# Kernel tuning notes

Measured on AMD Instinct MI355X. Metric: run time of the kernel, lower is better.

## Reference

```python
import jax, jax.numpy as jnp
import numpy as np

EPS = 1e-8  # matches torch cosine_similarity eps


def setup_inputs() -> dict:
    key = jax.random.key(0)
    ks = jax.random.split(key, 8)
    B, D_IN, H, L = 256, 256, 256, 100000
    G = 5 * H  # (N_GATES + 1) * hidden_dim
    s_in = 1.0 / np.sqrt(D_IN)
    s_h = 1.0 / np.sqrt(H)
    return {
        "x_t": jax.random.normal(ks[0], (B, D_IN), jnp.float32),
        "h": jax.random.normal(ks[1], (B, H), jnp.float32),
        "c": jax.random.normal(ks[2], (B, H), jnp.float32),
        "W_i2h": jax.random.normal(ks[3], (G, D_IN), jnp.float32) * s_in,
        "b_i2h": jnp.zeros((G,), jnp.float32),
        "W_h2h": jax.random.normal(ks[4], (G, H), jnp.float32) * s_h,
        "b_h2h": jnp.zeros((G,), jnp.float32),
        "keys": jax.random.normal(ks[5], (L, D_IN), jnp.float32),
        "vals": jax.random.normal(ks[6], (L, H), jnp.float32),
    }


def _dnd_get_memory(q, keys, vals):
    # cosine similarity of each query against every stored key -> [B, L]
    qn = q / jnp.maximum(jnp.linalg.norm(q, axis=-1, keepdims=True), EPS)
    kn = keys / jnp.maximum(jnp.linalg.norm(keys, axis=-1, keepdims=True), EPS)
    sims = jnp.einsum("bd,ld->bl", qn, kn)
    w = jax.nn.softmax(sims, axis=-1)          # softmax-weighted aggregation
    return jnp.einsum("bl,lh->bh", w, vals)    # [B, H]


def reference(x_t, h, c, W_i2h, b_i2h, W_h2h, b_h2h, keys, vals):
    H = h.shape[1]
    preact = (x_t @ W_i2h.T + b_i2h) + (h @ W_h2h.T + b_h2h)   # [B, 5H]
    gates = jax.nn.sigmoid(preact[:, : 4 * H])
    f_t = gates[:, :H]
    i_t = gates[:, H:2 * H]
    o_t = gates[:, 2 * H:3 * H]
    r_t = gates[:, 3 * H:4 * H]
    c_t_new = jnp.tanh(preact[:, 4 * H:])
    c_t = f_t * c + i_t * c_t_new
    m_t = jnp.tanh(_dnd_get_memory(x_t, keys, vals))
    c_t = c_t + r_t * m_t
    h_t = o_t * jnp.tanh(c_t)
    return (h_t, c_t)
```

## Files before the change

### kernel.cpp

```cpp
#include <hip/hip_runtime.h>
#include <stdint.h>

typedef float f4_t __attribute__((ext_vector_type(4)));
typedef float f16_t __attribute__((ext_vector_type(16)));
typedef __bf16 bf8_t __attribute__((ext_vector_type(8)));
typedef unsigned short us4_t __attribute__((ext_vector_type(4)));
typedef unsigned short us8_t __attribute__((ext_vector_type(8)));

static __device__ __forceinline__ unsigned short fbf(float f) {
    __bf16 b = (__bf16)f;
    return *(unsigned short*)&b;
}
static __device__ __forceinline__ float bf2f(unsigned short u) {
    union { uint32_t u; float f; } v; v.u = ((uint32_t)u) << 16;
    return v.f;
}
static __device__ __forceinline__ f4_t mfma16(bf8_t a, bf8_t b, f4_t c) {
    return __builtin_amdgcn_mfma_f32_16x16x32_bf16(a, b, c, 0, 0, 0);
}
static __device__ __forceinline__ f16_t mfma32(bf8_t a, bf8_t b, f16_t c) {
    return __builtin_amdgcn_mfma_f32_32x32x16_bf16(a, b, c, 0, 0, 0);
}
static __device__ __forceinline__ float sigf(float x) {
    return 1.0f / (1.0f + __expf(-x));
}
static __device__ __forceinline__ void gload_lds16(const void* g, void* l) {
    __builtin_amdgcn_global_load_lds(
        (const __attribute__((address_space(1))) void*)g,
        (__attribute__((address_space(3))) void*)l, 16, 0, 0);
}
static __device__ __forceinline__ uint32_t cvtpk(float lo, float hi) {
    uint32_t r;
    asm("v_cvt_pk_bf16_f32 %0, %1, %2" : "=v"(r) : "v"(lo), "v"(hi));
    return r;
}

__global__ __launch_bounds__(256) void k_convert(
    const float* __restrict__ x, const float* __restrict__ h,
    const float* __restrict__ W1, const float* __restrict__ W2,
    unsigned short* __restrict__ qn, unsigned short* __restrict__ xb,
    unsigned short* __restrict__ hb, unsigned short* __restrict__ w1b,
    unsigned short* __restrict__ w2b)
{
    __shared__ float sred[4];
    int bid = blockIdx.x, t = threadIdx.x;
    if (bid < 256) {
        float v = x[bid * 256 + t];
        float ss = v * v;
        #pragma unroll
        for (int m = 1; m < 64; m <<= 1) ss += __shfl_xor(ss, m, 64);
        if ((t & 63) == 0) sred[t >> 6] = ss;
        __syncthreads();
        float tot = sred[0] + sred[1] + sred[2] + sred[3];
        float rn = 1.0f / fmaxf(sqrtf(tot), 1e-8f);
        xb[bid * 256 + t] = fbf(v);
        qn[bid * 256 + t] = fbf(v * rn);
    } else if (bid < 512) {
        int b = bid - 256;
        hb[b * 256 + t] = fbf(h[b * 256 + t]);
    } else {
        int i0 = (bid - 512) * 256 + t;
        for (int i = i0; i < 1280 * 256; i += 512 * 256) {
            w1b[i] = fbf(W1[i]);
            w2b[i] = fbf(W2[i]);
        }
    }
}

__global__ __launch_bounds__(256) void k_gates(
    const unsigned short* __restrict__ xb, const unsigned short* __restrict__ hb,
    const unsigned short* __restrict__ w1b, const unsigned short* __restrict__ w2b,
    const float* __restrict__ b1, const float* __restrict__ b2,
    float* __restrict__ pre)
{
    int bb = (blockIdx.x & 3) * 64;
    int gb = (blockIdx.x >> 2) * 64;
    int t = threadIdx.x, w = t >> 6, lane = t & 63;
    int l15 = lane & 15, q8 = (lane >> 4) * 8, q4 = (lane >> 4) * 4;
    int arow = bb + w * 16 + l15;

    f4_t acc[4] = {};
    #pragma unroll
    for (int ks = 0; ks < 8; ++ks) {
        bf8_t a = *(const bf8_t*)&xb[arow * 256 + ks * 32 + q8];
        #pragma unroll
        for (int gc = 0; gc < 4; ++gc) {
            bf8_t bf = *(const bf8_t*)&w1b[(gb + gc * 16 + l15) * 256 + ks * 32 + q8];
            acc[gc] = mfma16(a, bf, acc[gc]);
        }
    }
    #pragma unroll
    for (int ks = 0; ks < 8; ++ks) {
        bf8_t a = *(const bf8_t*)&hb[arow * 256 + ks * 32 + q8];
        #pragma unroll
        for (int gc = 0; gc < 4; ++gc) {
            bf8_t bf = *(const bf8_t*)&w2b[(gb + gc * 16 + l15) * 256 + ks * 32 + q8];
            acc[gc] = mfma16(a, bf, acc[gc]);
        }
    }
    #pragma unroll
    for (int gc = 0; gc < 4; ++gc) {
        int g = gb + gc * 16 + l15;
        float bias = b1[g] + b2[g];
        #pragma unroll
        for (int r = 0; r < 4; ++r) {
            int b = bb + w * 16 + q4 + r;
            pre[b * 1280 + g] = acc[gc][r] + bias;
        }
    }
}

__global__ __launch_bounds__(256, 2) void k_dnd(
    const float* __restrict__ keys, const float* __restrict__ vals,
    const unsigned short* __restrict__ qn,
    unsigned short* __restrict__ opart, float* __restrict__ dpart,
    int L, int CH)
{
    __shared__ __align__(16) char smem[76288];

    const int t = threadIdx.x;
    const int w = t >> 6, lane = t & 63;
    const int l31 = lane & 31, hi = lane >> 5;

    const int bid = blockIdx.x;
    const int xcd = bid & 7, sl = bid >> 3;
    const int var = sl & 3;
    const int hhalf = var & 1, bhalf = var >> 1;
    const int chunk = (sl >> 2) * 8 + xcd;
    const int base = chunk * CH;
    int nk = L - base;
    if (nk > CH) nk = CH;
    if (nk < 0) nk = 0;
    const int nt = (nk + 31) >> 5;

    bf8_t qf[16];
    #pragma unroll
    for (int st = 0; st < 16; ++st)
        qf[st] = *(const bf8_t*)&qn[(bhalf * 128 + w * 32 + l31) * 256 + st * 16 + hi * 8];

    f16_t o[4] = {};
    float den = 0.f;

    auto issueRaw = [&](int tt) {
        int r0 = base + tt * 32;
        #pragma unroll
        for (int i = 0; i < 8; ++i) {
            int lr = 8 * w + i;
            int row = r0 + lr;
            if (row >= L) row = L - 1;
            gload_lds16(keys + (size_t)row * 256 + lane * 4, smem + lr * 1040);
        }
        #pragma unroll
        for (int j = 0; j < 4; ++j) {
            int lr = 8 * w + 2 * j;
            int row = r0 + lr + hi;
            if (row >= L) row = L - 1;
            gload_lds16(vals + (size_t)row * 256 + hhalf * 128 + l31 * 4,
                        smem + 33280 + lr * 512);
        }
    };

    auto convert = [&]() {
        {
            const int r = t >> 3, j = t & 7;
            const char* rk = smem + r * 1040;
            f4_t x[8];
            #pragma unroll
            for (int k = 0; k < 8; ++k)
                x[k] = *(const f4_t*)(rk + j * 128 + k * 16);
            float ss = 0.f;
            #pragma unroll
            for (int k = 0; k < 8; ++k)
                ss += x[k][0]*x[k][0] + x[k][1]*x[k][1]
                    + x[k][2]*x[k][2] + x[k][3]*x[k][3];
            ss += __shfl_xor(ss, 1, 64);
            ss += __shfl_xor(ss, 2, 64);
            ss += __shfl_xor(ss, 4, 64);
            float rn = 1.0f / fmaxf(sqrtf(ss), 1e-8f);
            unsigned short* Kb = (unsigned short*)(smem + 49664);
            #pragma unroll
            for (int kk = 0; kk < 4; ++kk) {
                us8_t uv;
                #pragma unroll
                for (int e = 0; e < 4; ++e) {
                    uv[e]     = fbf(x[2*kk][e] * rn);
                    uv[e + 4] = fbf(x[2*kk + 1][e] * rn);
                }
                int col = j * 64 + kk * 16;
                *(us8_t*)((char*)Kb + r * 512 + (col ^ ((r & 7) * 16))) = uv;
            }
        }
        {
            const float* rv = (const float*)(smem + 33280);
            unsigned short* Vb = (unsigned short*)(smem + 66048);
            #pragma unroll
            for (int hh2 = 0; hh2 < 2; ++hh2) {
                int hh = lane + hh2 * 64;
                us8_t uv;
                #pragma unroll
                for (int i = 0; i < 8; ++i)
                    uv[i] = fbf(rv[(8 * w + i) * 128 + hh]);
                *(us8_t*)&Vb[hh * 40 + 8 * w] = uv;
            }
        }
    };

    const unsigned short* Kb = (const unsigned short*)(smem + 49664);
    const unsigned short* Vb = (const unsigned short*)(smem + 66048);

    if (nt > 0) {
        issueRaw(0);
        asm volatile("s_waitcnt vmcnt(0)" ::: "memory");
        convert();
        if (nt > 1) issueRaw(1);
        asm volatile("s_waitcnt lgkmcnt(0)\n\ts_barrier" ::: "memory");

        for (int tt = 0; tt < nt; ++tt) {
            f16_t sc = {};
            __builtin_amdgcn_s_setprio(1);
            #pragma unroll
            for (int st = 0; st < 16; ++st) {
                bf8_t kf = *(const bf8_t*)((const char*)Kb + l31 * 512 +
                               ((st * 32 + hi * 16) ^ ((l31 & 7) * 16)));
                sc = mfma32(kf, qf[st], sc);
            }
            __builtin_amdgcn_s_setprio(0);

            float p[16];
            bool full = (tt * 32 + 32 <= nk);
            #pragma unroll
            for (int r = 0; r < 16; ++r) {
                int l = (r & 3) + 8 * (r >> 2) + 4 * hi;
                float pv = __expf(sc[r] - 1.0f);
                if (!full && (tt * 32 + l) >= nk) pv = 0.f;
                p[r] = pv;
                den += pv;
            }
            uint32_t a0 = cvtpk(p[0], p[1]),   a1 = cvtpk(p[2], p[3]);
            uint32_t b0 = cvtpk(p[4], p[5]),   b1 = cvtpk(p[6], p[7]);
            uint32_t c0 = cvtpk(p[8], p[9]),   c1 = cvtpk(p[10], p[11]);
            uint32_t d0 = cvtpk(p[12], p[13]), d1 = cvtpk(p[14], p[15]);
            asm("v_permlane32_swap_b32 %0, %1" : "+v"(a0), "+v"(b0));
            asm("v_permlane32_swap_b32 %0, %1" : "+v"(a1), "+v"(b1));
            asm("v_permlane32_swap_b32 %0, %1" : "+v"(c0), "+v"(d0));
            asm("v_permlane32_swap_b32 %0, %1" : "+v"(c1), "+v"(d1));
            union { uint32_t u[4]; bf8_t v; } pa0, pa1;
            pa0.u[0] = a0; pa0.u[1] = a1; pa0.u[2] = b0; pa0.u[3] = b1;
            pa1.u[0] = c0; pa1.u[1] = c1; pa1.u[2] = d0; pa1.u[3] = d1;

            __builtin_amdgcn_s_setprio(1);
            #pragma unroll
            for (int g = 0; g < 4; ++g) {
                bf8_t vf0 = *(const bf8_t*)&Vb[(g * 32 + l31) * 40 + hi * 8];
                bf8_t vf1 = *(const bf8_t*)&Vb[(g * 32 + l31) * 40 + 16 + hi * 8];
                o[g] = mfma32(pa0.v, vf0, o[g]);
                o[g] = mfma32(pa1.v, vf1, o[g]);
            }
            __builtin_amdgcn_s_setprio(0);

            if (tt + 1 < nt) {
                asm volatile("s_waitcnt vmcnt(0)" ::: "memory");
                __builtin_amdgcn_s_barrier();
                convert();
                if (tt + 2 < nt) issueRaw(tt + 2);
                asm volatile("s_waitcnt lgkmcnt(0)\n\ts_barrier" ::: "memory");
            }
        }
    }

    asm volatile("s_waitcnt vmcnt(0)" ::: "memory");
    __syncthreads();
    unsigned short* Ol = (unsigned short*)smem;
    #pragma unroll
    for (int g = 0; g < 4; ++g)
        #pragma unroll
        for (int r = 0; r < 16; ++r) {
            int b = w * 32 + (r & 3) + 8 * (r >> 2) + 4 * hi;
            Ol[b * 128 + g * 32 + l31] = fbf(o[g][r]);
        }
    __syncthreads();
    {
        size_t ob = (size_t)((chunk * 2 + bhalf) * 2 + hhalf) * 16384;
        #pragma unroll
        for (int it = 0; it < 8; ++it) {
            int off = it * 2048 + t * 8;
            *(us8_t*)&opart[ob + off] = *(const us8_t*)&Ol[off];
        }
    }
    den += __shfl_xor(den, 32, 64);
    if (hi == 0 && hhalf == 0)
        dpart[chunk * 256 + bhalf * 128 + w * 32 + l31] = den;
}

__global__ __launch_bounds__(256) void k_reduce(
    const unsigned short* __restrict__ opart, const float* __restrict__ dpart,
    const float* __restrict__ pre, const float* __restrict__ c_in,
    float* __restrict__ out)
{
    __shared__ float sred[4];
    int b = blockIdx.x, t = threadIdx.x;

    float ds = dpart[t * 256 + b];
    #pragma unroll
    for (int m = 1; m < 64; m <<= 1) ds += __shfl_xor(ds, m, 64);
    if ((t & 63) == 0) sred[t >> 6] = ds;
    __syncthreads();
    float dtot = fmaxf(sred[0] + sred[1] + sred[2] + sred[3], 1e-30f);

    int bh = b >> 7, br = b & 127;
    int hh = t >> 7, hc = t & 127;
    size_t sb = (size_t)(bh * 2 + hh) * 16384 + br * 128 + hc;
    float n0 = 0.f, n1 = 0.f, n2 = 0.f, n3 = 0.f;
    for (int ck = 0; ck < 256; ck += 4) {
        n0 += bf2f(opart[(size_t)(ck + 0) * 65536 + sb]);
        n1 += bf2f(opart[(size_t)(ck + 1) * 65536 + sb]);
        n2 += bf2f(opart[(size_t)(ck + 2) * 65536 + sb]);
        n3 += bf2f(opart[(size_t)(ck + 3) * 65536 + sb]);
    }
    float num = (n0 + n1) + (n2 + n3);

    float m = tanhf(num / dtot);
    const float* p = pre + b * 1280;
    float fg = sigf(p[t]);
    float ig = sigf(p[256 + t]);
    float og = sigf(p[512 + t]);
    float rg = sigf(p[768 + t]);
    float cn = tanhf(p[1024 + t]);
    float co = c_in[b * 256 + t];
    float ct = fg * co + ig * cn + rg * m;
    float ht = og * tanhf(ct);
    out[b * 256 + t] = ht;
    out[65536 + b * 256 + t] = ct;
}

extern "C" void kernel_launch(void* const* d_in, const int* in_sizes, int n_in,
                              void* d_out, int out_size, void* d_ws, size_t ws_size,
                              hipStream_t stream)
{
    const float* x    = (const float*)d_in[0];
    const float* h    = (const float*)d_in[1];
    const float* c    = (const float*)d_in[2];
    const float* W1   = (const float*)d_in[3];
    const float* b1   = (const float*)d_in[4];
    const float* W2   = (const float*)d_in[5];
    const float* b2   = (const float*)d_in[6];
    const float* keys = (const float*)d_in[7];
    const float* vals = (const float*)d_in[8];
    int L = in_sizes[7] / 256;

    int TILES = (L + 256 * 32 - 1) / (256 * 32);
    int CH = TILES * 32;

    char* ws = (char*)d_ws;
    unsigned short* qn    = (unsigned short*)(ws + 0);
    unsigned short* xb    = (unsigned short*)(ws + 131072);
    unsigned short* hb    = (unsigned short*)(ws + 262144);
    unsigned short* w1b   = (unsigned short*)(ws + 393216);
    unsigned short* w2b   = (unsigned short*)(ws + 1048576);
    float*          pre   = (float*)(ws + 1703936);
    float*          dpart = (float*)(ws + 3014656);
    unsigned short* opart = (unsigned short*)(ws + 3276800);

    k_convert<<<dim3(1024), dim3(256), 0, stream>>>(x, h, W1, W2, qn, xb, hb, w1b, w2b);
    k_gates<<<dim3(80), dim3(256), 0, stream>>>(xb, hb, w1b, w2b, b1, b2, pre);
    k_dnd<<<dim3(1024), dim3(256), 0, stream>>>(keys, vals, qn, opart, dpart, L, CH);
    k_reduce<<<dim3(256), dim3(256), 0, stream>>>(opart, dpart, pre, c, (float*)d_out);

    (void)n_in; (void)out_size; (void)ws_size;
}
```

Measured before the change: 119.3 us.

## Prenormalize keys to bf16 in a separate pass and drop H-split in DND

Adds a k_prep kernel that normalizes keys and writes them as swizzled bf16 tiles to workspace. k_dnd then streams those tiles straight into double-buffered LDS and loads vals through registers with a split prefetch placed around the score MFMAs. Each block now covers the full 256-wide H instead of half, so the grid is halved and each key tile is read once per batch half rather than twice. The cost is an extra kernel launch plus a bf16 key write and re-read, more accumulator registers, and a different opart layout in the reduce.

```diff
diff --git a/kernel.cpp b/kernel.cpp
--- a/kernel.cpp
+++ b/kernel.cpp
@@ -110,121 +110,145 @@
     }
 }
 
+__global__ __launch_bounds__(256) void k_prep(
+    const float* __restrict__ keys, unsigned short* __restrict__ kn,
+    int L, int CH, int TILES)
+{
+    int gt = blockIdx.x;
+    int chunk = gt / TILES, tile = gt - chunk * TILES;
+    int t = threadIdx.x;
+    int r = t >> 3, j = t & 7;
+    int grow = chunk * CH + tile * 32 + r;
+
+    f4_t x[8];
+    if (grow < L) {
+        const float* src = keys + (size_t)grow * 256 + j * 32;
+        #pragma unroll
+        for (int k = 0; k < 8; ++k) x[k] = *(const f4_t*)(src + 4 * k);
+    } else {
+        #pragma unroll
+        for (int k = 0; k < 8; ++k) x[k] = f4_t{0.f, 0.f, 0.f, 0.f};
+    }
+    float ss = 0.f;
+    #pragma unroll
+    for (int k = 0; k < 8; ++k)
+        ss += x[k][0]*x[k][0] + x[k][1]*x[k][1] + x[k][2]*x[k][2] + x[k][3]*x[k][3];
+    ss += __shfl_xor(ss, 1, 64);
+    ss += __shfl_xor(ss, 2, 64);
+    ss += __shfl_xor(ss, 4, 64);
+    float rn = 1.0f / fmaxf(sqrtf(ss), 1e-8f);
+
+    char* dst = (char*)kn + (size_t)gt * 16384 + r * 512;
+    #pragma unroll
+    for (int k2 = 0; k2 < 4; ++k2) {
+        us8_t uv;
+        #pragma unroll
+        for (int e = 0; e < 4; ++e) {
+            uv[e]     = fbf(x[2*k2][e] * rn);
+            uv[e + 4] = fbf(x[2*k2 + 1][e] * rn);
+        }
+        *(us8_t*)(dst + ((j * 64 + k2 * 16) ^ (r * 16))) = uv;
+    }
+}
+
 __global__ __launch_bounds__(256, 2) void k_dnd(
-    const float* __restrict__ keys, const float* __restrict__ vals,
+    const float* __restrict__ vals, const unsigned short* __restrict__ kn,
     const unsigned short* __restrict__ qn,
     unsigned short* __restrict__ opart, float* __restrict__ dpart,
-    int L, int CH)
-{
-    __shared__ __align__(16) char smem[76288];
+    int L, int CH, int TILES)
+{
+    __shared__ __align__(16) char smem[71680];
+    char* Vb = smem + 32768;
 
     const int t = threadIdx.x;
     const int w = t >> 6, lane = t & 63;
     const int l31 = lane & 31, hi = lane >> 5;
 
     const int bid = blockIdx.x;
-    const int xcd = bid & 7, sl = bid >> 3;
-    const int var = sl & 3;
-    const int hhalf = var & 1, bhalf = var >> 1;
-    const int chunk = (sl >> 2) * 8 + xcd;
+    const int xcd = bid & 7;
+    const int idx = bid >> 3;
+    const int bhalf = idx & 1;
+    const int chunk = (idx >> 1) * 8 + xcd;
     const int base = chunk * CH;
     int nk = L - base;
     if (nk > CH) nk = CH;
     if (nk < 0) nk = 0;
     const int nt = (nk + 31) >> 5;
 
+    const int hcol = l31 + 32 * (w * 2 + hi);
+
     bf8_t qf[16];
     #pragma unroll
     for (int st = 0; st < 16; ++st)
         qf[st] = *(const bf8_t*)&qn[(bhalf * 128 + w * 32 + l31) * 256 + st * 16 + hi * 8];
 
-    f16_t o[4] = {};
+    f16_t o[8] = {};
     float den = 0.f;
-
-    auto issueRaw = [&](int tt) {
+    float vst[32];
+
+    auto issueK = [&](int tt) {
+        const char* src = (const char*)kn + (size_t)(chunk * TILES + tt) * 16384
+                        + w * 4096 + lane * 16;
+        char* dst = smem + (tt & 1) * 16384 + w * 4096;
+        #pragma unroll
+        for (int c = 0; c < 4; ++c)
+            gload_lds16(src + c * 1024, dst + c * 1024);
+    };
+    auto issueVa = [&](int tt) {
         int r0 = base + tt * 32;
         #pragma unroll
-        for (int i = 0; i < 8; ++i) {
-            int lr = 8 * w + i;
-            int row = r0 + lr;
+        for (int r = 0; r < 16; ++r) {
+            int row = r0 + r;
             if (row >= L) row = L - 1;
-            gload_lds16(keys + (size_t)row * 256 + lane * 4, smem + lr * 1040);
-        }
-        #pragma unroll
-        for (int j = 0; j < 4; ++j) {
-            int lr = 8 * w + 2 * j;
-            int row = r0 + lr + hi;
+            vst[r] = *(volatile const float*)&vals[(size_t)row * 256 + hcol];
+        }
+    };
+    auto issueVb = [&](int tt) {
+        int r0 = base + tt * 32;
+        #pragma unroll
+        for (int r = 16; r < 32; ++r) {
+            int row = r0 + r;
             if (row >= L) row = L - 1;
-            gload_lds16(vals + (size_t)row * 256 + hhalf * 128 + l31 * 4,
-                        smem + 33280 + lr * 512);
+            vst[r] = *(volatile const float*)&vals[(size_t)row * 256 + hcol];
         }
     };
-
-    auto convert = [&]() {
-        {
-            const int r = t >> 3, j = t & 7;
-            const char* rk = smem + r * 1040;
-            f4_t x[8];
-            #pragma unroll
-            for (int k = 0; k < 8; ++k)
-                x[k] = *(const f4_t*)(rk + j * 128 + k * 16);
-            float ss = 0.f;
-            #pragma unroll
-            for (int k = 0; k < 8; ++k)
-                ss += x[k][0]*x[k][0] + x[k][1]*x[k][1]
-                    + x[k][2]*x[k][2] + x[k][3]*x[k][3];
-            ss += __shfl_xor(ss, 1, 64);
-            ss += __shfl_xor(ss, 2, 64);
-            ss += __shfl_xor(ss, 4, 64);
-            float rn = 1.0f / fmaxf(sqrtf(ss), 1e-8f);
-            unsigned short* Kb = (unsigned short*)(smem + 49664);
-            #pragma unroll
-            for (int kk = 0; kk < 4; ++kk) {
-                us8_t uv;
-                #pragma unroll
-                for (int e = 0; e < 4; ++e) {
-                    uv[e]     = fbf(x[2*kk][e] * rn);
-                    uv[e + 4] = fbf(x[2*kk + 1][e] * rn);
-                }
-                int col = j * 64 + kk * 16;
-                *(us8_t*)((char*)Kb + r * 512 + (col ^ ((r & 7) * 16))) = uv;
-            }
-        }
-        {
-            const float* rv = (const float*)(smem + 33280);
-            unsigned short* Vb = (unsigned short*)(smem + 66048);
-            #pragma unroll
-            for (int hh2 = 0; hh2 < 2; ++hh2) {
-                int hh = lane + hh2 * 64;
-                us8_t uv;
-                #pragma unroll
-                for (int i = 0; i < 8; ++i)
-                    uv[i] = fbf(rv[(8 * w + i) * 128 + hh]);
-                *(us8_t*)&Vb[hh * 40 + 8 * w] = uv;
-            }
+    auto convertV = [&]() {
+        #pragma unroll
+        for (int q = 0; q < 8; ++q) {
+            union { uint32_t u[2]; us4_t s; } pv;
+            pv.u[0] = cvtpk(vst[4*q],     vst[4*q + 1]);
+            pv.u[1] = cvtpk(vst[4*q + 2], vst[4*q + 3]);
+            *(us4_t*)(Vb + hcol * 152 + q * 8) = pv.s;
         }
     };
 
-    const unsigned short* Kb = (const unsigned short*)(smem + 49664);
-    const unsigned short* Vb = (const unsigned short*)(smem + 66048);
-
     if (nt > 0) {
-        issueRaw(0);
+        issueK(0);
+        issueVa(0); issueVb(0);
         asm volatile("s_waitcnt vmcnt(0)" ::: "memory");
-        convert();
-        if (nt > 1) issueRaw(1);
+        convertV();
+        issueK(nt > 1 ? 1 : 0);
         asm volatile("s_waitcnt lgkmcnt(0)\n\ts_barrier" ::: "memory");
 
         for (int tt = 0; tt < nt; ++tt) {
+            int tn = tt + 1 < nt ? tt + 1 : nt - 1;
+            issueVa(tn);
+            __builtin_amdgcn_sched_barrier(0);
+
+            const char* Kb = smem + (tt & 1) * 16384;
+
             f16_t sc = {};
             __builtin_amdgcn_s_setprio(1);
             #pragma unroll
             for (int st = 0; st < 16; ++st) {
-                bf8_t kf = *(const bf8_t*)((const char*)Kb + l31 * 512 +
-                               ((st * 32 + hi * 16) ^ ((l31 & 7) * 16)));
+                bf8_t kf = *(const bf8_t*)(Kb + l31 * 512 +
+                               (((2 * st + hi) * 16) ^ (l31 * 16)));
                 sc = mfma32(kf, qf[st], sc);
             }
             __builtin_amdgcn_s_setprio(0);
+
+            issueVb(tn);
+            __builtin_amdgcn_sched_barrier(0);
 
             float p[16];
             bool full = (tt * 32 + 32 <= nk);
@@ -250,19 +274,24 @@
 
             __builtin_amdgcn_s_setprio(1);
             #pragma unroll
-            for (int g = 0; g < 4; ++g) {
-                bf8_t vf0 = *(const bf8_t*)&Vb[(g * 32 + l31) * 40 + hi * 8];
-                bf8_t vf1 = *(const bf8_t*)&Vb[(g * 32 + l31) * 40 + 16 + hi * 8];
-                o[g] = mfma32(pa0.v, vf0, o[g]);
-                o[g] = mfma32(pa1.v, vf1, o[g]);
+            for (int g = 0; g < 8; ++g) {
+                const char* vb = Vb + (g * 32 + l31) * 152 + hi * 16;
+                union { us4_t h[2]; bf8_t v; } vf0, vf1;
+                vf0.h[0] = *(const us4_t*)(vb);
+                vf0.h[1] = *(const us4_t*)(vb + 8);
+                vf1.h[0] = *(const us4_t*)(vb + 32);
+                vf1.h[1] = *(const us4_t*)(vb + 40);
+                o[g] = mfma32(pa0.v, vf0.v, o[g]);
+                o[g] = mfma32(pa1.v, vf1.v, o[g]);
             }
             __builtin_amdgcn_s_setprio(0);
 
+            asm volatile("s_waitcnt lgkmcnt(0)\n\ts_barrier" ::: "memory");
+
             if (tt + 1 < nt) {
                 asm volatile("s_waitcnt vmcnt(0)" ::: "memory");
-                __builtin_amdgcn_s_barrier();
-                convert();
-                if (tt + 2 < nt) issueRaw(tt + 2);
+                convertV();
+                issueK(tt + 2 < nt ? tt + 2 : nt - 1);
                 asm volatile("s_waitcnt lgkmcnt(0)\n\ts_barrier" ::: "memory");
             }
         }
@@ -272,23 +301,23 @@
     __syncthreads();
     unsigned short* Ol = (unsigned short*)smem;
     #pragma unroll
-    for (int g = 0; g < 4; ++g)
+    for (int g = 0; g < 8; ++g)
         #pragma unroll
         for (int r = 0; r < 16; ++r) {
             int b = w * 32 + (r & 3) + 8 * (r >> 2) + 4 * hi;
-            Ol[b * 128 + g * 32 + l31] = fbf(o[g][r]);
+            Ol[b * 256 + g * 32 + l31] = fbf(o[g][r]);
         }
     __syncthreads();
     {
-        size_t ob = (size_t)((chunk * 2 + bhalf) * 2 + hhalf) * 16384;
-        #pragma unroll
-        for (int it = 0; it < 8; ++it) {
+        size_t ob = (size_t)(chunk * 2 + bhalf) * 32768;
+        #pragma unroll
+        for (int it = 0; it < 16; ++it) {
             int off = it * 2048 + t * 8;
             *(us8_t*)&opart[ob + off] = *(const us8_t*)&Ol[off];
         }
     }
     den += __shfl_xor(den, 32, 64);
-    if (hi == 0 && hhalf == 0)
+    if (hi == 0)
         dpart[chunk * 256 + bhalf * 128 + w * 32 + l31] = den;
 }
 
@@ -308,14 +337,13 @@
     float dtot = fmaxf(sred[0] + sred[1] + sred[2] + sred[3], 1e-30f);
 
     int bh = b >> 7, br = b & 127;
-    int hh = t >> 7, hc = t & 127;
-    size_t sb = (size_t)(bh * 2 + hh) * 16384 + br * 128 + hc;
+    size_t sb = (size_t)br * 256 + t;
     float n0 = 0.f, n1 = 0.f, n2 = 0.f, n3 = 0.f;
     for (int ck = 0; ck < 256; ck += 4) {
-        n0 += bf2f(opart[(size_t)(ck + 0) * 65536 + sb]);
-        n1 += bf2f(opart[(size_t)(ck + 1) * 65536 + sb]);
-        n2 += bf2f(opart[(size_t)(ck + 2) * 65536 + sb]);
-        n3 += bf2f(opart[(size_t)(ck + 3) * 65536 + sb]);
+        n0 += bf2f(opart[(size_t)((ck + 0) * 2 + bh) * 32768 + sb]);
+        n1 += bf2f(opart[(size_t)((ck + 1) * 2 + bh) * 32768 + sb]);
+        n2 += bf2f(opart[(size_t)((ck + 2) * 2 + bh) * 32768 + sb]);
+        n3 += bf2f(opart[(size_t)((ck + 3) * 2 + bh) * 32768 + sb]);
     }
     float num = (n0 + n1) + (n2 + n3);
 
@@ -359,11 +387,13 @@
     unsigned short* w2b   = (unsigned short*)(ws + 1048576);
     float*          pre   = (float*)(ws + 1703936);
     float*          dpart = (float*)(ws + 3014656);
-    unsigned short* opart = (unsigned short*)(ws + 3276800);
+    unsigned short* kn    = (unsigned short*)(ws + 3276800);
+    unsigned short* opart = (unsigned short*)(ws + 3276800 + (size_t)256 * TILES * 16384);
 
     k_convert<<<dim3(1024), dim3(256), 0, stream>>>(x, h, W1, W2, qn, xb, hb, w1b, w2b);
     k_gates<<<dim3(80), dim3(256), 0, stream>>>(xb, hb, w1b, w2b, b1, b2, pre);
-    k_dnd<<<dim3(1024), dim3(256), 0, stream>>>(keys, vals, qn, opart, dpart, L, CH);
+    k_prep<<<dim3(256 * TILES), dim3(256), 0, stream>>>(keys, kn, L, CH, TILES);
+    k_dnd<<<dim3(512), dim3(256), 0, stream>>>(vals, kn, qn, opart, dpart, L, CH, TILES);
     k_reduce<<<dim3(256), dim3(256), 0, stream>>>(opart, dpart, pre, c, (float*)d_out);
 
     (void)n_in; (void)out_size; (void)ws_size;
```

Measured after the change: 305.8 us. +156.4%, slower.
